# Optimization experiments

Measured on AMD Instinct MI355X. Metric: run time of the kernel, lower is better.

Reference implementation:

```python
import jax, jax.numpy as jnp
import numpy as np

N = 100000
E = 1600000
B = 4
IN_C, HID_C, OUT_C = 128, 16, 64
EPS = 1e-5


def _xavier(key, shape):
    fan_in, fan_out = shape[0], shape[1]
    a = float(np.sqrt(6.0 / (fan_in + fan_out)))
    return jax.random.uniform(key, shape, jnp.float32, -a, a)


def setup_inputs() -> dict:
    key = jax.random.key(0)
    ks = jax.random.split(key, 12)
    return {
        "X": jax.random.normal(ks[0], (B, N, IN_C), jnp.float32),
        "edge_index0": jax.random.randint(ks[1], (2, E), 0, N, jnp.int32),
        "edge_weight0": jax.random.uniform(ks[2], (E,), jnp.float32),
        "edge_index1": jax.random.randint(ks[3], (2, E), 0, N, jnp.int32),
        "edge_weight1": jax.random.uniform(ks[4], (E,), jnp.float32),
        "n_id": jnp.arange(N, dtype=jnp.int32),
        "res_n_id0": jnp.arange(N, dtype=jnp.int32),
        "res_n_id1": jnp.arange(N, dtype=jnp.int32),
        # layer 1 params
        "W1_1": _xavier(ks[5], (IN_C, HID_C)),
        "W2_1": _xavier(ks[6], (1, HID_C)),
        "U1": _xavier(ks[7], (HID_C, HID_C)),
        "V1": _xavier(ks[8], (HID_C, HID_C)),
        # layer 2 params
        "W1_2": _xavier(ks[9], (HID_C, OUT_C)),
        "W2_2": _xavier(ks[10], (1, OUT_C)),
        "U2": _xavier(ks[11], (OUT_C, OUT_C)),
        "V2": _xavier(jax.random.fold_in(key, 99), (OUT_C, OUT_C)),
    }


def gated_gcn(x, edge_index, edge_weight, res_n_id, W1, W2, U, V, n_dst):
    # x: [B, N_src, C_in]
    x = x @ W1                                   # [B, N_src, C]
    edge_emb = edge_weight[:, None] * W2[0]      # [E, C]  (edge_feature @ W2)
    src, dst = edge_index[0], edge_index[1]
    msg = edge_emb[None, :, :] * (x[:, src, :] @ V)          # [B, E, C]
    # scatter-mean over destination nodes
    sums = jax.ops.segment_sum(jnp.swapaxes(msg, 0, 1), dst,
                               num_segments=n_dst)            # [N_dst, B, C]
    cnt = jax.ops.segment_sum(jnp.ones((msg.shape[1],), msg.dtype), dst,
                              num_segments=n_dst)
    aggr = jnp.swapaxes(sums, 0, 1) / jnp.maximum(cnt, 1.0)[None, :, None]
    # update
    xr = x[:, res_n_id, :]                       # [B, N_dst, C]
    a = xr @ U + aggr
    # fresh BatchNorm1d(num_features=N_dst) in train mode: normalize each
    # node index over (batch, channel); affine is identity (gamma=1, beta=0)
    mean = jnp.mean(a, axis=(0, 2), keepdims=True)
    var = jnp.var(a, axis=(0, 2), keepdims=True)
    a = jax.nn.relu((a - mean) * jax.lax.rsqrt(var + EPS))
    return xr + a


def reference(X, edge_index0, edge_weight0, edge_index1, edge_weight1,
              n_id, res_n_id0, res_n_id1,
              W1_1, W2_1, U1, V1, W1_2, W2_2, U2, V2):
    X = X[:, n_id, :]
    X = gated_gcn(X, edge_index0, edge_weight0, res_n_id0,
                  W1_1, W2_1, U1, V1, N)
    X = gated_gcn(X, edge_index1, edge_weight1, res_n_id1,
                  W1_2, W2_2, U2, V2, N)
    return X
```

## Files before the change

kernel.cpp:

```cpp
#include <hip/hip_runtime.h>

#define NN 100000
#define EE 1600000
#define EPS 1e-5f
#define NBUK 391
#define NB1 782
#define K1B 6250

typedef __attribute__((ext_vector_type(8))) short short8;
typedef __attribute__((ext_vector_type(4))) float floatx4;
union FragU { uint u[4]; short8 s; };

__device__ __forceinline__ ushort f2bf(float f) {
    uint u = __float_as_uint(f);
    uint r = (u + 0x7FFF + ((u >> 16) & 1)) >> 16;
    return (ushort)r;
}
__device__ __forceinline__ float bf2f(ushort u) {
    return __uint_as_float(((uint)u) << 16);
}

__global__ __launch_bounds__(256) void kA(const float* __restrict__ X,
                                          const float* __restrict__ W1_1,
                                          ushort* __restrict__ x1g,
                                          const int* __restrict__ ei0,
                                          const int* __restrict__ ei1,
                                          int* __restrict__ bh) {
    __shared__ __align__(16) char smem[64 * 132 * 4 + 4096];
    int t = threadIdx.x;
    if (blockIdx.x >= K1B) {
        int bp = blockIdx.x - K1B;
        int l = bp >= NB1;
        int b = bp - l * NB1;
        const int* dst = (l ? ei1 : ei0) + EE;
        int* hist = (int*)smem;
        for (int i = t; i < NBUK; i += 256) hist[i] = 0;
        __syncthreads();
        long base = (long)b * 2048;
#pragma unroll
        for (int k = 0; k < 8; ++k) {
            long i = base + k * 256 + t;
            if (i < EE) atomicAdd(&hist[dst[i] >> 8], 1);
        }
        __syncthreads();
        int* bhl = bh + (long)l * NBUK * NB1;
        for (int h = t; h < NBUK; h += 256) bhl[h * NB1 + b] = hist[h];
        return;
    }
    float (*Xs)[132] = (float(*)[132])smem;
    ushort* Ws = (ushort*)(smem + 64 * 132 * 4);
    int w = t >> 6, lane = t & 63;
    int nb = blockIdx.x * 16;
    for (int i = t; i < 2048; i += 256) {
        int e = i & 7, l = (i >> 3) & 63, s = i >> 9;
        Ws[i] = f2bf(W1_1[(s * 32 + ((l >> 4) & 3) * 8 + e) * 16 + (l & 15)]);
    }
#pragma unroll
    for (int i = 0; i < 8; ++i) {
        int flat = i * 256 + t;
        int n_loc = flat >> 7;
        int b = (flat >> 5) & 3;
        int c4 = (flat & 31) << 2;
        float4 v = *reinterpret_cast<const float4*>(&X[((long)b * NN + (nb + n_loc)) * 128 + c4]);
        *reinterpret_cast<float4*>(&Xs[n_loc * 4 + b][c4]) = v;
    }
    __syncthreads();
    int arow = lane & 15, q = lane >> 4;
    floatx4 acc = {0.f, 0.f, 0.f, 0.f};
#pragma unroll
    for (int s = 0; s < 4; ++s) {
        const float* xp = &Xs[w * 16 + arow][s * 32 + q * 8];
        float4 xa = *reinterpret_cast<const float4*>(xp);
        float4 xb = *reinterpret_cast<const float4*>(xp + 4);
        FragU a;
        a.u[0] = ((uint)f2bf(xa.y) << 16) | f2bf(xa.x);
        a.u[1] = ((uint)f2bf(xa.w) << 16) | f2bf(xa.z);
        a.u[2] = ((uint)f2bf(xb.y) << 16) | f2bf(xb.x);
        a.u[3] = ((uint)f2bf(xb.w) << 16) | f2bf(xb.z);
        short8 bfrag = *reinterpret_cast<const short8*>(&Ws[(s * 64 + lane) * 8]);
        acc = __builtin_amdgcn_mfma_f32_16x16x32_bf16(a.s, bfrag, acc, 0, 0, 0);
    }
    int nw = nb + w * 4;
#pragma unroll
    for (int r = 0; r < 4; ++r) {
        int i = q * 4 + r;
        x1g[(long)(nw + (i >> 2)) * 64 + (i & 3) * 16 + (lane & 15)] = f2bf(acc[r]);
    }
}

__global__ __launch_bounds__(256) void passB(int* __restrict__ bh, int* __restrict__ colsum) {
    int l = blockIdx.x >= NBUK;
    int h = blockIdx.x - l * NBUK;
    int* row = bh + ((long)l * NBUK + h) * NB1;
    int t = threadIdx.x;
    int v[4];
    int s = 0;
    int b0 = t * 4;
#pragma unroll
    for (int j = 0; j < 4; ++j) {
        int b = b0 + j;
        int x = (b < NB1) ? row[b] : 0;
        v[j] = x;
        s += x;
    }
    int lane = t & 63, wv = t >> 6;
    int x = s;
#pragma unroll
    for (int off = 1; off < 64; off <<= 1) {
        int y = __shfl_up(x, off, 64);
        if (lane >= off) x += y;
    }
    __shared__ int wsum[4], wpre[4];
    if (lane == 63) wsum[wv] = x;
    __syncthreads();
    if (t == 0) {
        int ss = 0;
        for (int i = 0; i < 4; ++i) { wpre[i] = ss; ss += wsum[i]; }
    }
    __syncthreads();
    int run = wpre[wv] + x - s;
#pragma unroll
    for (int j = 0; j < 4; ++j) {
        int b = b0 + j;
        if (b < NB1) row[b] = run;
        run += v[j];
    }
    if (t == 255) colsum[l * NBUK + h] = run;
}

__global__ __launch_bounds__(256) void gbscan(const int* __restrict__ colsum, int* __restrict__ gb,
                                              const float* __restrict__ W1_2,
                                              const float* __restrict__ U2,
                                              const float* __restrict__ V2,
                                              const float* __restrict__ W2_2,
                                              const float* __restrict__ U1,
                                              const float* __restrict__ V1,
                                              const float* __restrict__ W2_1,
                                              ushort* __restrict__ pack5a,
                                              ushort* __restrict__ pack5b,
                                              ushort* __restrict__ pack3,
                                              int2* __restrict__ ecsr0, int2* __restrict__ ecsr1,
                                              int* __restrict__ rp0, int* __restrict__ rp1) {
    int t = threadIdx.x;
    if (blockIdx.x == 3) {
        for (int i = t; i < 512; i += 256) {
            int e = i & 7, l = i >> 3;
            int kk = ((l >> 4) & 3) * 8 + e, h = l & 15;
            float v = (kk < 16) ? U1[kk * 16 + h] : V1[(kk - 16) * 16 + h] * W2_1[h];
            pack3[i] = f2bf(v);
        }
        return;
    }
    if (blockIdx.x == 2) {
        for (int i = t; i < 1024; i += 256) {
            int k = i >> 6, j = i & 63;
            float su = 0.f, sv = 0.f;
            for (int m = 0; m < 64; ++m) {
                float wm = W1_2[k * 64 + m];
                su += wm * U2[m * 64 + j];
                sv += wm * V2[m * 64 + j];
            }
            sv *= W2_2[j];
            int jt = j >> 4;
            int l1 = (k >> 3) * 16 + (j & 15);
            int l2 = (2 + (k >> 3)) * 16 + (j & 15);
            int e = k & 7;
            pack5a[(jt * 64 + l1) * 8 + e] = f2bf(su);
            pack5a[(jt * 64 + l2) * 8 + e] = f2bf(sv);
            pack5b[(jt * 64 + l1) * 8 + e] = f2bf(W1_2[k * 64 + j]);
            pack5b[(jt * 64 + l2) * 8 + e] = 0;
        }
        if (t < 16) { ecsr0[EE + t] = make_int2(0, 0); ecsr1[EE + t] = make_int2(0, 0); }
        if (t == 16) rp0[NN] = EE;
        if (t == 17) rp1[NN] = EE;
        return;
    }
    int l = blockIdx.x;
    const int* cs = colsum + l * NBUK;
    int v[2];
    int s = 0;
#pragma unroll
    for (int j = 0; j < 2; ++j) {
        int i = t * 2 + j;
        int x = (i < NBUK) ? cs[i] : 0;
        v[j] = x;
        s += x;
    }
    int lane = t & 63, wv = t >> 6;
    int x = s;
#pragma unroll
    for (int off = 1; off < 64; off <<= 1) {
        int y = __shfl_up(x, off, 64);
        if (lane >= off) x += y;
    }
    __shared__ int wsum[4], wpre[4];
    if (lane == 63) wsum[wv] = x;
    __syncthreads();
    if (t == 0) {
        int ss = 0;
        for (int i = 0; i < 4; ++i) { wpre[i] = ss; ss += wsum[i]; }
    }
    __syncthreads();
    int run = wpre[wv] + x - s;
    int* g = gb + l * 392;
#pragma unroll
    for (int j = 0; j < 2; ++j) {
        int i = t * 2 + j;
        if (i < NBUK) g[i] = run;
        run += v[j];
    }
    if (t == 255) g[NBUK] = run;
}

__global__ __launch_bounds__(256) void passC(const int* __restrict__ ei0, const float* __restrict__ ew0,
                                             const int* __restrict__ ei1, const float* __restrict__ ew1,
                                             const int* __restrict__ bh, const int* __restrict__ gb,
                                             int2* __restrict__ tmp) {
    int l = blockIdx.x >= NB1;
    int b = blockIdx.x - l * NB1;
    const int* ei = l ? ei1 : ei0;
    const float* ew = l ? ew1 : ew0;
    const int* dst = ei + EE;
    __shared__ int cur[NBUK];
    int t = threadIdx.x;
    const int* bhl = bh + (long)l * NBUK * NB1;
    const int* gbl = gb + l * 392;
    for (int h = t; h < NBUK; h += 256) cur[h] = gbl[h] + bhl[h * NB1 + b];
    __syncthreads();
    long base = (long)b * 2048;
    int2* tl = tmp + (long)l * EE;
#pragma unroll
    for (int k = 0; k < 8; ++k) {
        long i = base + k * 256 + t;
        if (i < EE) {
            int d = dst[i];
            int slot = atomicAdd(&cur[d >> 8], 1);
            tl[slot] = make_int2(ei[i] | ((d & 255) << 17), __float_as_int(ew[i]));
        }
    }
}

__global__ __launch_bounds__(256) void passD(const int* __restrict__ gb,
                                             const int2* __restrict__ tmp,
                                             int2* __restrict__ ecsr0, int2* __restrict__ ecsr1,
                                             int* __restrict__ rp0, int* __restrict__ rp1) {
    int l = blockIdx.x >= NBUK;
    int h = blockIdx.x - l * NBUK;
    const int* gbl = gb + l * 392;
    int base = gbl[h], size = gbl[h + 1] - base;
    const int2* tl = tmp + (long)l * EE;
    int2* ecsr = l ? ecsr1 : ecsr0;
    int* rp = l ? rp1 : rp0;
    __shared__ int2 stage[6400];
    __shared__ int hist[256];
    __shared__ int wsum[4], wpre[4];
    int t = threadIdx.x;
    hist[t] = 0;
    __syncthreads();
    bool fit = (size <= 6400);
    for (int i = t; i < size; i += 256) {
        int2 r = tl[base + i];
        if (fit) stage[i] = r;
        atomicAdd(&hist[(r.x >> 17) & 255], 1);
    }
    __syncthreads();
    int v = hist[t];
    int lane = t & 63, wv = t >> 6;
    int x = v;
#pragma unroll
    for (int off = 1; off < 64; off <<= 1) {
        int y = __shfl_up(x, off, 64);
        if (lane >= off) x += y;
    }
    if (lane == 63) wsum[wv] = x;
    __syncthreads();
    if (t == 0) {
        int ss = 0;
        for (int i = 0; i < 4; ++i) { wpre[i] = ss; ss += wsum[i]; }
    }
    __syncthreads();
    int excl = wpre[wv] + x - v;
    int node = h * 256 + t;
    if (node < NN) rp[node] = base + excl;
    __syncthreads();
    hist[t] = excl;
    __syncthreads();
    for (int i = t; i < size; i += 256) {
        int2 r = fit ? stage[i] : tl[base + i];
        int L = (r.x >> 17) & 255;
        int slot = base + atomicAdd(&hist[L], 1);
        ecsr[slot] = make_int2((r.x & 0x1FFFF) << 7, r.y);
    }
}

__global__ __launch_bounds__(256) void k3(const ushort* __restrict__ x1g,
                                          const int2* __restrict__ ecsr0,
                                          const int* __restrict__ rp0,
                                          const ushort* __restrict__ pack3,
                                          ushort* __restrict__ h1g) {
    __shared__ ushort xg[4][16][40];
    int t = threadIdx.x;
    int w = t >> 6, lane = t & 63;
    int b = lane >> 4;
    int nb = blockIdx.x * 16 + w * 4;
    const char* xb = (const char*)x1g;
    int lb = lane << 1;
    int s0 = rp0[nb], b1 = rp0[nb + 1], b2 = rp0[nb + 2], b3 = rp0[nb + 3], s4 = rp0[nb + 4];
    float acc0 = 0.f, acc1 = 0.f, acc2 = 0.f, acc3 = 0.f;
    for (int e = s0; e < s4; e += 16) {
        int2 r[16];
#pragma unroll
        for (int i = 0; i < 16; ++i) r[i] = ecsr0[e + i];
        float v[16];
#pragma unroll
        for (int i = 0; i < 16; ++i)
            v[i] = bf2f(*(const ushort*)(xb + (uint)r[i].x + lb));
#pragma unroll
        for (int i = 0; i < 16; ++i) {
            int gi = e + i;
            float wm = (gi < s4) ? __int_as_float(r[i].y) : 0.f;
            float c = wm * v[i];
            acc0 += (gi < b1) ? c : 0.f;
            acc1 += (gi >= b1 && gi < b2) ? c : 0.f;
            acc2 += (gi >= b2 && gi < b3) ? c : 0.f;
            acc3 += (gi >= b3) ? c : 0.f;
        }
    }
    int h = lane & 15;
    xg[w][0 * 4 + b][16 + h] = f2bf(acc0 / fmaxf((float)(b1 - s0), 1.f));
    xg[w][1 * 4 + b][16 + h] = f2bf(acc1 / fmaxf((float)(b2 - b1), 1.f));
    xg[w][2 * 4 + b][16 + h] = f2bf(acc2 / fmaxf((float)(b3 - b2), 1.f));
    xg[w][3 * 4 + b][16 + h] = f2bf(acc3 / fmaxf((float)(s4 - b3), 1.f));
#pragma unroll
    for (int j = 0; j < 4; ++j)
        xg[w][j * 4 + b][h] = x1g[(long)(nb + j) * 64 + lane];
    short8 afrag = *reinterpret_cast<const short8*>(&xg[w][lane & 15][(lane >> 4) * 8]);
    short8 bfrag = *reinterpret_cast<const short8*>(&pack3[lane * 8]);
    floatx4 a4 = {0.f, 0.f, 0.f, 0.f};
    a4 = __builtin_amdgcn_mfma_f32_16x16x32_bf16(afrag, bfrag, a4, 0, 0, 0);
    float s = 0.f, s2 = 0.f;
#pragma unroll
    for (int r = 0; r < 4; ++r) { s += a4[r]; s2 += a4[r] * a4[r]; }
#pragma unroll
    for (int off = 1; off <= 8; off <<= 1) {
        s += __shfl_xor(s, off, 64);
        s2 += __shfl_xor(s2, off, 64);
    }
    float mean = s * (1.f / 64.f);
    float var = s2 * (1.f / 64.f) - mean * mean;
    float rs = rsqrtf(var + EPS);
    int node = lane >> 4;
#pragma unroll
    for (int r = 0; r < 4; ++r) {
        float xv = bf2f(xg[w][node * 4 + r][lane & 15]);
        float hv = xv + fmaxf((a4[r] - mean) * rs, 0.f);
        h1g[(long)(nb + node) * 64 + r * 16 + (lane & 15)] = f2bf(hv);
    }
}

__global__ __launch_bounds__(256) void k5(const ushort* __restrict__ h1g,
                                          const int2* __restrict__ ecsr1,
                                          const int* __restrict__ rp1,
                                          const ushort* __restrict__ pack5a,
                                          const ushort* __restrict__ pack5b,
                                          float* __restrict__ out) {
    __shared__ ushort hg[4][16][40];
    int t = threadIdx.x;
    int w = t >> 6, lane = t & 63;
    int b = lane >> 4;
    int nb = blockIdx.x * 16 + w * 4;
    const char* hb = (const char*)h1g;
    int lb = lane << 1;
    int s0 = rp1[nb], b1 = rp1[nb + 1], b2 = rp1[nb + 2], b3 = rp1[nb + 3], s4 = rp1[nb + 4];
    float acc0 = 0.f, acc1 = 0.f, acc2 = 0.f, acc3 = 0.f;
    for (int e = s0; e < s4; e += 16) {
        int2 r[16];
#pragma unroll
        for (int i = 0; i < 16; ++i) r[i] = ecsr1[e + i];
        float v[16];
#pragma unroll
        for (int i = 0; i < 16; ++i)
            v[i] = bf2f(*(const ushort*)(hb + (uint)r[i].x + lb));
#pragma unroll
        for (int i = 0; i < 16; ++i) {
            int gi = e + i;
            float wm = (gi < s4) ? __int_as_float(r[i].y) : 0.f;
            float c = wm * v[i];
            acc0 += (gi < b1) ? c : 0.f;
            acc1 += (gi >= b1 && gi < b2) ? c : 0.f;
            acc2 += (gi >= b2 && gi < b3) ? c : 0.f;
            acc3 += (gi >= b3) ? c : 0.f;
        }
    }
    int h = lane & 15;
    hg[w][0 * 4 + b][16 + h] = f2bf(acc0 / fmaxf((float)(b1 - s0), 1.f));
    hg[w][1 * 4 + b][16 + h] = f2bf(acc1 / fmaxf((float)(b2 - b1), 1.f));
    hg[w][2 * 4 + b][16 + h] = f2bf(acc2 / fmaxf((float)(b3 - b2), 1.f));
    hg[w][3 * 4 + b][16 + h] = f2bf(acc3 / fmaxf((float)(s4 - b3), 1.f));
#pragma unroll
    for (int j = 0; j < 4; ++j)
        hg[w][j * 4 + b][h] = h1g[(long)(nb + j) * 64 + lane];
    short8 afrag = *reinterpret_cast<const short8*>(&hg[w][lane & 15][(lane >> 4) * 8]);
    floatx4 c1[4], c2[4];
#pragma unroll
    for (int jt = 0; jt < 4; ++jt) {
        short8 bb1 = *reinterpret_cast<const short8*>(&pack5a[(jt * 64 + lane) * 8]);
        short8 bb2 = *reinterpret_cast<const short8*>(&pack5b[(jt * 64 + lane) * 8]);
        floatx4 z = {0.f, 0.f, 0.f, 0.f};
        c1[jt] = __builtin_amdgcn_mfma_f32_16x16x32_bf16(afrag, bb1, z, 0, 0, 0);
        c2[jt] = __builtin_amdgcn_mfma_f32_16x16x32_bf16(afrag, bb2, z, 0, 0, 0);
    }
    float s = 0.f, s2 = 0.f;
#pragma unroll
    for (int jt = 0; jt < 4; ++jt)
#pragma unroll
        for (int r = 0; r < 4; ++r) { float a = c1[jt][r]; s += a; s2 += a * a; }
#pragma unroll
    for (int off = 1; off <= 8; off <<= 1) {
        s += __shfl_xor(s, off, 64);
        s2 += __shfl_xor(s2, off, 64);
    }
    float mean = s * (1.f / 256.f);
    float var = s2 * (1.f / 256.f) - mean * mean;
    float rs = rsqrtf(var + EPS);
    int node = lane >> 4;
    long n = nb + node;
#pragma unroll
    for (int r = 0; r < 4; ++r)
#pragma unroll
        for (int jt = 0; jt < 4; ++jt) {
            float norm = (c1[jt][r] - mean) * rs;
            out[((long)r * NN + n) * 64 + jt * 16 + (lane & 15)] = c2[jt][r] + fmaxf(norm, 0.f);
        }
}

extern "C" void kernel_launch(void* const* d_in, const int* in_sizes, int n_in,
                              void* d_out, int out_size, void* d_ws, size_t ws_size,
                              hipStream_t stream) {
    const float* X    = (const float*)d_in[0];
    const int*   ei0  = (const int*)d_in[1];
    const float* ew0  = (const float*)d_in[2];
    const int*   ei1  = (const int*)d_in[3];
    const float* ew1  = (const float*)d_in[4];
    const float* W1_1 = (const float*)d_in[8];
    const float* W2_1 = (const float*)d_in[9];
    const float* U1   = (const float*)d_in[10];
    const float* V1   = (const float*)d_in[11];
    const float* W1_2 = (const float*)d_in[12];
    const float* W2_2 = (const float*)d_in[13];
    const float* U2   = (const float*)d_in[14];
    const float* V2   = (const float*)d_in[15];
    float* out = (float*)d_out;
    char* ws = (char*)d_ws;

    const long MB = 1000000L;
    ushort* x1g   = (ushort*)(ws + 0L);
    ushort* h1g   = (ushort*)(ws + 13 * MB);
    int2*   tmp   = (int2*)(ws + 26 * MB);
    int*    bh    = (int*)(ws + 52 * MB);
    int*    colsum= (int*)(ws + 55 * MB);
    int*    gb    = (int*)(ws + 55 * MB + 4096);
    int*    rp0   = (int*)(ws + 56 * MB);
    int*    rp1   = (int*)(ws + 57 * MB);
    int2*   ecsr0 = (int2*)(ws + 58 * MB);
    int2*   ecsr1 = (int2*)(ws + 71 * MB);
    ushort* pack3  = (ushort*)(ws + 84 * MB);
    ushort* pack5a = (ushort*)(ws + 84 * MB + 8192);
    ushort* pack5b = (ushort*)(ws + 84 * MB + 16384);

    kA<<<K1B + 2 * NB1, 256, 0, stream>>>(X, W1_1, x1g, ei0, ei1, bh);
    passB<<<2 * NBUK, 256, 0, stream>>>(bh, colsum);
    gbscan<<<4, 256, 0, stream>>>(colsum, gb, W1_2, U2, V2, W2_2, U1, V1, W2_1,
                                  pack5a, pack5b, pack3, ecsr0, ecsr1, rp0, rp1);
    passC<<<2 * NB1, 256, 0, stream>>>(ei0, ew0, ei1, ew1, bh, gb, tmp);
    passD<<<2 * NBUK, 256, 0, stream>>>(gb, tmp, ecsr0, ecsr1, rp0, rp1);
    k3<<<K1B, 256, 0, stream>>>(x1g, ecsr0, rp0, pack3, h1g);
    k5<<<K1B, 256, 0, stream>>>(h1g, ecsr1, rp1, pack5a, pack5b, out);
}
```

Measured before the change: 328.1 us.

## Stagger layer-1 CSR build across layer-0 passes and fused compute kernels

Weight packing moves from gbscan into extra blocks of kA. The layer-1 edge scatter (passC) now runs in the same launch as the layer-0 bucket sort (passD), and the layer-1 bucket sort runs in the same launch as the layer-0 aggregation kernel k3. The aim is to let independent work from the two layers overlap and to remove launch gaps. In exchange, passD no longer stages edges in LDS, so it reads tmp twice from global memory, and the fused kernels mix block types with different resource needs.

```diff
diff --git a/kernel.cpp b/kernel.cpp
--- a/kernel.cpp
+++ b/kernel.cpp
@@ -20,14 +20,121 @@
     return __uint_as_float(((uint)u) << 16);
 }
 
+__device__ __forceinline__ int blockScanExcl(int v, int* wsum, int* wpre) {
+    int t = threadIdx.x, lane = t & 63, wv = t >> 6;
+    int x = v;
+#pragma unroll
+    for (int off = 1; off < 64; off <<= 1) {
+        int y = __shfl_up(x, off, 64);
+        if (lane >= off) x += y;
+    }
+    if (lane == 63) wsum[wv] = x;
+    __syncthreads();
+    if (t == 0) {
+        int ss = 0;
+        for (int i = 0; i < 4; ++i) { wpre[i] = ss; ss += wsum[i]; }
+    }
+    __syncthreads();
+    return wpre[wv] + x - v;
+}
+
+__device__ __forceinline__ void passC_body(const int* __restrict__ ei, const float* __restrict__ ew,
+                                           const int* __restrict__ bhl, const int* __restrict__ gbl,
+                                           int2* __restrict__ tl, int b, int* cur) {
+    const int* dst = ei + EE;
+    int t = threadIdx.x;
+    for (int h = t; h < NBUK; h += 256) cur[h] = gbl[h] + bhl[h * NB1 + b];
+    __syncthreads();
+    long base = (long)b * 2048;
+#pragma unroll
+    for (int k = 0; k < 8; ++k) {
+        long i = base + k * 256 + t;
+        if (i < EE) {
+            int d = dst[i];
+            int slot = atomicAdd(&cur[d >> 8], 1);
+            tl[slot] = make_int2(ei[i] | ((d & 255) << 17), __float_as_int(ew[i]));
+        }
+    }
+}
+
+__device__ __forceinline__ void passD_body(const int* __restrict__ gbl, const int2* __restrict__ tl,
+                                           int2* __restrict__ ecsr, int* __restrict__ rp,
+                                           int h, int* hist, int* wsum, int* wpre) {
+    int t = threadIdx.x;
+    int base = gbl[h], size = gbl[h + 1] - base;
+    hist[t] = 0;
+    __syncthreads();
+    for (int i = t; i < size; i += 256)
+        atomicAdd(&hist[(tl[base + i].x >> 17) & 255], 1);
+    __syncthreads();
+    int v = hist[t];
+    int excl = blockScanExcl(v, wsum, wpre);
+    int node = h * 256 + t;
+    if (node < NN) rp[node] = base + excl;
+    __syncthreads();
+    hist[t] = excl;
+    __syncthreads();
+    for (int i = t; i < size; i += 256) {
+        int2 r = tl[base + i];
+        int L = (r.x >> 17) & 255;
+        int slot = base + atomicAdd(&hist[L], 1);
+        ecsr[slot] = make_int2((r.x & 0x1FFFF) << 7, r.y);
+    }
+}
+
 __global__ __launch_bounds__(256) void kA(const float* __restrict__ X,
                                           const float* __restrict__ W1_1,
                                           ushort* __restrict__ x1g,
                                           const int* __restrict__ ei0,
                                           const int* __restrict__ ei1,
-                                          int* __restrict__ bh) {
+                                          int* __restrict__ bh,
+                                          const float* __restrict__ W1_2,
+                                          const float* __restrict__ U2,
+                                          const float* __restrict__ V2,
+                                          const float* __restrict__ W2_2,
+                                          const float* __restrict__ U1,
+                                          const float* __restrict__ V1,
+                                          const float* __restrict__ W2_1,
+                                          ushort* __restrict__ pack5a,
+                                          ushort* __restrict__ pack5b,
+                                          ushort* __restrict__ pack3,
+                                          int2* __restrict__ ecsr0, int2* __restrict__ ecsr1,
+                                          int* __restrict__ rp0, int* __restrict__ rp1) {
     __shared__ __align__(16) char smem[64 * 132 * 4 + 4096];
     int t = threadIdx.x;
+    if (blockIdx.x >= K1B + 2 * NB1) {
+        if (blockIdx.x == K1B + 2 * NB1) {
+            for (int i = t; i < 1024; i += 256) {
+                int k = i >> 6, j = i & 63;
+                float su = 0.f, sv = 0.f;
+                for (int m = 0; m < 64; ++m) {
+                    float wm = W1_2[k * 64 + m];
+                    su += wm * U2[m * 64 + j];
+                    sv += wm * V2[m * 64 + j];
+                }
+                sv *= W2_2[j];
+                int jt = j >> 4;
+                int l1 = (k >> 3) * 16 + (j & 15);
+                int l2 = (2 + (k >> 3)) * 16 + (j & 15);
+                int e = k & 7;
+                pack5a[(jt * 64 + l1) * 8 + e] = f2bf(su);
+                pack5a[(jt * 64 + l2) * 8 + e] = f2bf(sv);
+                pack5b[(jt * 64 + l1) * 8 + e] = f2bf(W1_2[k * 64 + j]);
+                pack5b[(jt * 64 + l2) * 8 + e] = 0;
+            }
+            if (t < 16) { ecsr0[EE + t] = make_int2(0, 0); ecsr1[EE + t] = make_int2(0, 0); }
+            if (t == 16) rp0[NN] = EE;
+            if (t == 17) rp1[NN] = EE;
+        } else {
+            for (int i = t; i < 512; i += 256) {
+                int e = i & 7, l = i >> 3;
+                int kk = ((l >> 4) & 3) * 8 + e, h = l & 15;
+                float v = (kk < 16) ? U1[kk * 16 + h] : V1[(kk - 16) * 16 + h] * W2_1[h];
+                pack3[i] = f2bf(v);
+            }
+        }
+        return;
+    }
     if (blockIdx.x >= K1B) {
         int bp = blockIdx.x - K1B;
         int l = bp >= NB1;
@@ -103,22 +210,8 @@
         v[j] = x;
         s += x;
     }
-    int lane = t & 63, wv = t >> 6;
-    int x = s;
-#pragma unroll
-    for (int off = 1; off < 64; off <<= 1) {
-        int y = __shfl_up(x, off, 64);
-        if (lane >= off) x += y;
-    }
     __shared__ int wsum[4], wpre[4];
-    if (lane == 63) wsum[wv] = x;
-    __syncthreads();
-    if (t == 0) {
-        int ss = 0;
-        for (int i = 0; i < 4; ++i) { wpre[i] = ss; ss += wsum[i]; }
-    }
-    __syncthreads();
-    int run = wpre[wv] + x - s;
+    int run = blockScanExcl(s, wsum, wpre);
 #pragma unroll
     for (int j = 0; j < 4; ++j) {
         int b = b0 + j;
@@ -128,54 +221,9 @@
     if (t == 255) colsum[l * NBUK + h] = run;
 }
 
-__global__ __launch_bounds__(256) void gbscan(const int* __restrict__ colsum, int* __restrict__ gb,
-                                              const float* __restrict__ W1_2,
-                                              const float* __restrict__ U2,
-                                              const float* __restrict__ V2,
-                                              const float* __restrict__ W2_2,
-                                              const float* __restrict__ U1,
-                                              const float* __restrict__ V1,
-                                              const float* __restrict__ W2_1,
-                                              ushort* __restrict__ pack5a,
-                                              ushort* __restrict__ pack5b,
-                                              ushort* __restrict__ pack3,
-                                              int2* __restrict__ ecsr0, int2* __restrict__ ecsr1,
-                                              int* __restrict__ rp0, int* __restrict__ rp1) {
-    int t = threadIdx.x;
-    if (blockIdx.x == 3) {
-        for (int i = t; i < 512; i += 256) {
-            int e = i & 7, l = i >> 3;
-            int kk = ((l >> 4) & 3) * 8 + e, h = l & 15;
-            float v = (kk < 16) ? U1[kk * 16 + h] : V1[(kk - 16) * 16 + h] * W2_1[h];
-            pack3[i] = f2bf(v);
-        }
-        return;
-    }
-    if (blockIdx.x == 2) {
-        for (int i = t; i < 1024; i += 256) {
-            int k = i >> 6, j = i & 63;
-            float su = 0.f, sv = 0.f;
-            for (int m = 0; m < 64; ++m) {
-                float wm = W1_2[k * 64 + m];
-                su += wm * U2[m * 64 + j];
-                sv += wm * V2[m * 64 + j];
-            }
-            sv *= W2_2[j];
-            int jt = j >> 4;
-            int l1 = (k >> 3) * 16 + (j & 15);
-            int l2 = (2 + (k >> 3)) * 16 + (j & 15);
-            int e = k & 7;
-            pack5a[(jt * 64 + l1) * 8 + e] = f2bf(su);
-            pack5a[(jt * 64 + l2) * 8 + e] = f2bf(sv);
-            pack5b[(jt * 64 + l1) * 8 + e] = f2bf(W1_2[k * 64 + j]);
-            pack5b[(jt * 64 + l2) * 8 + e] = 0;
-        }
-        if (t < 16) { ecsr0[EE + t] = make_int2(0, 0); ecsr1[EE + t] = make_int2(0, 0); }
-        if (t == 16) rp0[NN] = EE;
-        if (t == 17) rp1[NN] = EE;
-        return;
-    }
+__global__ __launch_bounds__(256) void gbscan(const int* __restrict__ colsum, int* __restrict__ gb) {
     int l = blockIdx.x;
+    int t = threadIdx.x;
     const int* cs = colsum + l * NBUK;
     int v[2];
     int s = 0;
@@ -186,22 +234,8 @@
         v[j] = x;
         s += x;
     }
-    int lane = t & 63, wv = t >> 6;
-    int x = s;
-#pragma unroll
-    for (int off = 1; off < 64; off <<= 1) {
-        int y = __shfl_up(x, off, 64);
-        if (lane >= off) x += y;
-    }
     __shared__ int wsum[4], wpre[4];
-    if (lane == 63) wsum[wv] = x;
-    __syncthreads();
-    if (t == 0) {
-        int ss = 0;
-        for (int i = 0; i < 4; ++i) { wpre[i] = ss; ss += wsum[i]; }
-    }
-    __syncthreads();
-    int run = wpre[wv] + x - s;
+    int run = blockScanExcl(s, wsum, wpre);
     int* g = gb + l * 392;
 #pragma unroll
     for (int j = 0; j < 2; ++j) {
@@ -212,97 +246,37 @@
     if (t == 255) g[NBUK] = run;
 }
 
-__global__ __launch_bounds__(256) void passC(const int* __restrict__ ei0, const float* __restrict__ ew0,
-                                             const int* __restrict__ ei1, const float* __restrict__ ew1,
-                                             const int* __restrict__ bh, const int* __restrict__ gb,
-                                             int2* __restrict__ tmp) {
-    int l = blockIdx.x >= NB1;
-    int b = blockIdx.x - l * NB1;
-    const int* ei = l ? ei1 : ei0;
-    const float* ew = l ? ew1 : ew0;
-    const int* dst = ei + EE;
+__global__ __launch_bounds__(256) void passC0(const int* __restrict__ ei0, const float* __restrict__ ew0,
+                                              const int* __restrict__ bh, const int* __restrict__ gb,
+                                              int2* __restrict__ tmp) {
     __shared__ int cur[NBUK];
-    int t = threadIdx.x;
-    const int* bhl = bh + (long)l * NBUK * NB1;
-    const int* gbl = gb + l * 392;
-    for (int h = t; h < NBUK; h += 256) cur[h] = gbl[h] + bhl[h * NB1 + b];
-    __syncthreads();
-    long base = (long)b * 2048;
-    int2* tl = tmp + (long)l * EE;
-#pragma unroll
-    for (int k = 0; k < 8; ++k) {
-        long i = base + k * 256 + t;
-        if (i < EE) {
-            int d = dst[i];
-            int slot = atomicAdd(&cur[d >> 8], 1);
-            tl[slot] = make_int2(ei[i] | ((d & 255) << 17), __float_as_int(ew[i]));
-        }
-    }
-}
-
-__global__ __launch_bounds__(256) void passD(const int* __restrict__ gb,
-                                             const int2* __restrict__ tmp,
-                                             int2* __restrict__ ecsr0, int2* __restrict__ ecsr1,
-                                             int* __restrict__ rp0, int* __restrict__ rp1) {
-    int l = blockIdx.x >= NBUK;
-    int h = blockIdx.x - l * NBUK;
-    const int* gbl = gb + l * 392;
-    int base = gbl[h], size = gbl[h + 1] - base;
-    const int2* tl = tmp + (long)l * EE;
-    int2* ecsr = l ? ecsr1 : ecsr0;
-    int* rp = l ? rp1 : rp0;
-    __shared__ int2 stage[6400];
-    __shared__ int hist[256];
+    passC_body(ei0, ew0, bh, gb, tmp, blockIdx.x, cur);
+}
+
+__global__ __launch_bounds__(256) void fuseDC(const int* __restrict__ gb, int2* __restrict__ tmp,
+                                              int2* __restrict__ ecsr0, int* __restrict__ rp0,
+                                              const int* __restrict__ ei1, const float* __restrict__ ew1,
+                                              const int* __restrict__ bh) {
+    __shared__ int sh[NBUK];
     __shared__ int wsum[4], wpre[4];
-    int t = threadIdx.x;
-    hist[t] = 0;
-    __syncthreads();
-    bool fit = (size <= 6400);
-    for (int i = t; i < size; i += 256) {
-        int2 r = tl[base + i];
-        if (fit) stage[i] = r;
-        atomicAdd(&hist[(r.x >> 17) & 255], 1);
-    }
-    __syncthreads();
-    int v = hist[t];
-    int lane = t & 63, wv = t >> 6;
-    int x = v;
-#pragma unroll
-    for (int off = 1; off < 64; off <<= 1) {
-        int y = __shfl_up(x, off, 64);
-        if (lane >= off) x += y;
-    }
-    if (lane == 63) wsum[wv] = x;
-    __syncthreads();
-    if (t == 0) {
-        int ss = 0;
-        for (int i = 0; i < 4; ++i) { wpre[i] = ss; ss += wsum[i]; }
-    }
-    __syncthreads();
-    int excl = wpre[wv] + x - v;
-    int node = h * 256 + t;
-    if (node < NN) rp[node] = base + excl;
-    __syncthreads();
-    hist[t] = excl;
-    __syncthreads();
-    for (int i = t; i < size; i += 256) {
-        int2 r = fit ? stage[i] : tl[base + i];
-        int L = (r.x >> 17) & 255;
-        int slot = base + atomicAdd(&hist[L], 1);
-        ecsr[slot] = make_int2((r.x & 0x1FFFF) << 7, r.y);
-    }
-}
-
-__global__ __launch_bounds__(256) void k3(const ushort* __restrict__ x1g,
-                                          const int2* __restrict__ ecsr0,
-                                          const int* __restrict__ rp0,
-                                          const ushort* __restrict__ pack3,
-                                          ushort* __restrict__ h1g) {
-    __shared__ ushort xg[4][16][40];
+    if (blockIdx.x < NBUK) {
+        passD_body(gb, tmp, ecsr0, rp0, blockIdx.x, sh, wsum, wpre);
+    } else {
+        passC_body(ei1, ew1, bh + (long)NBUK * NB1, gb + 392, tmp + (long)EE,
+                   blockIdx.x - NBUK, sh);
+    }
+}
+
+__device__ __forceinline__ void k3_body(const ushort* __restrict__ x1g,
+                                        const int2* __restrict__ ecsr0,
+                                        const int* __restrict__ rp0,
+                                        const ushort* __restrict__ pack3,
+                                        ushort* __restrict__ h1g,
+                                        ushort (*xg)[16][40], int blk) {
     int t = threadIdx.x;
     int w = t >> 6, lane = t & 63;
     int b = lane >> 4;
-    int nb = blockIdx.x * 16 + w * 4;
+    int nb = blk * 16 + w * 4;
     const char* xb = (const char*)x1g;
     int lb = lane << 1;
     int s0 = rp0[nb], b1 = rp0[nb + 1], b2 = rp0[nb + 2], b3 = rp0[nb + 3], s4 = rp0[nb + 4];
@@ -355,6 +329,25 @@
         float xv = bf2f(xg[w][node * 4 + r][lane & 15]);
         float hv = xv + fmaxf((a4[r] - mean) * rs, 0.f);
         h1g[(long)(nb + node) * 64 + r * 16 + (lane & 15)] = f2bf(hv);
+    }
+}
+
+__global__ __launch_bounds__(256) void fuseKD(const ushort* __restrict__ x1g,
+                                              const int2* __restrict__ ecsr0,
+                                              const int* __restrict__ rp0,
+                                              const ushort* __restrict__ pack3,
+                                              ushort* __restrict__ h1g,
+                                              const int* __restrict__ gb,
+                                              const int2* __restrict__ tmp,
+                                              int2* __restrict__ ecsr1,
+                                              int* __restrict__ rp1) {
+    __shared__ ushort xg[4][16][40];
+    __shared__ int hist[256];
+    __shared__ int wsum[4], wpre[4];
+    if (blockIdx.x < K1B) {
+        k3_body(x1g, ecsr0, rp0, pack3, h1g, xg, blockIdx.x);
+    } else {
+        passD_body(gb + 392, tmp + (long)EE, ecsr1, rp1, blockIdx.x - K1B, hist, wsum, wpre);
     }
 }
 
@@ -468,12 +461,13 @@
     ushort* pack5a = (ushort*)(ws + 84 * MB + 8192);
     ushort* pack5b = (ushort*)(ws + 84 * MB + 16384);
 
-    kA<<<K1B + 2 * NB1, 256, 0, stream>>>(X, W1_1, x1g, ei0, ei1, bh);
+    kA<<<K1B + 2 * NB1 + 2, 256, 0, stream>>>(X, W1_1, x1g, ei0, ei1, bh,
+                                              W1_2, U2, V2, W2_2, U1, V1, W2_1,
+                                              pack5a, pack5b, pack3, ecsr0, ecsr1, rp0, rp1);
     passB<<<2 * NBUK, 256, 0, stream>>>(bh, colsum);
-    gbscan<<<4, 256, 0, stream>>>(colsum, gb, W1_2, U2, V2, W2_2, U1, V1, W2_1,
-                                  pack5a, pack5b, pack3, ecsr0, ecsr1, rp0, rp1);
-    passC<<<2 * NB1, 256, 0, stream>>>(ei0, ew0, ei1, ew1, bh, gb, tmp);
-    passD<<<2 * NBUK, 256, 0, stream>>>(gb, tmp, ecsr0, ecsr1, rp0, rp1);
-    k3<<<K1B, 256, 0, stream>>>(x1g, ecsr0, rp0, pack3, h1g);
+    gbscan<<<2, 256, 0, stream>>>(colsum, gb);
+    passC0<<<NB1, 256, 0, stream>>>(ei0, ew0, bh, gb, tmp);
+    fuseDC<<<NBUK + NB1, 256, 0, stream>>>(gb, tmp, ecsr0, rp0, ei1, ew1, bh);
+    fuseKD<<<K1B + NBUK, 256, 0, stream>>>(x1g, ecsr0, rp0, pack3, h1g, gb, tmp, ecsr1, rp1);
     k5<<<K1B, 256, 0, stream>>>(h1g, ecsr1, rp1, pack5a, pack5b, out);
 }
```

Result: faster. 307.1 us (-6.4%).
